# Performance work log

Hardware: AMD Instinct MI355X
Metric: run time of the kernel (lower is better)

The kernel has to match this reference:

```python
import jax, jax.numpy as jnp
import numpy as np

HEADS = 4
DIM_HEAD = 64
SCALE = 10.0
EPS = 1e-12  # matches torch F.normalize default eps


def setup_inputs() -> dict:
    key = jax.random.key(0)
    k1, k2, k3, k4, k5 = jax.random.split(key, 5)
    dim = 256
    hidden = HEADS * DIM_HEAD
    x = jax.random.normal(k1, (16, dim, 32, 32), dtype=jnp.float32)
    y = jax.random.normal(k2, (16, dim, 32, 32), dtype=jnp.float32)
    # 1x1 conv weights stored as 2D matrices (out_ch, in_ch)
    w_qkv = jax.random.normal(k3, (hidden * 3, dim), dtype=jnp.float32) * (1.0 / np.sqrt(dim))
    w_out = jax.random.normal(k4, (dim, hidden), dtype=jnp.float32) * (1.0 / np.sqrt(hidden))
    b_out = jax.random.normal(k5, (dim,), dtype=jnp.float32) * 0.01
    return {"x": x, "y": y, "w_qkv": w_qkv, "w_out": w_out, "b_out": b_out}


def _l2norm(t):
    # torch F.normalize(t, dim=-1): t / max(||t||_2, eps)
    n = jnp.sqrt(jnp.sum(t * t, axis=-1, keepdims=True))
    return t / jnp.maximum(n, EPS)


def reference(x, y, w_qkv, w_out, b_out):
    b, c, hh, ww = x.shape
    n_x = hh * ww
    n_y = y.shape[2] * y.shape[3]
    hidden = HEADS * DIM_HEAD

    # 1x1 convs == channel matmuls; only q from x and k,v from y are used
    w_q, w_k, w_v = w_qkv[:hidden], w_qkv[hidden:2 * hidden], w_qkv[2 * hidden:]
    q = jnp.einsum('oc,bcn->bon', w_q, x.reshape(b, c, n_x)).reshape(b, HEADS, DIM_HEAD, n_x)
    k = jnp.einsum('oc,bcn->bon', w_k, y.reshape(b, c, n_y)).reshape(b, HEADS, DIM_HEAD, n_y)
    v = jnp.einsum('oc,bcn->bon', w_v, y.reshape(b, c, n_y)).reshape(b, HEADS, DIM_HEAD, n_y)

    # l2norm over the spatial (last) axis, as in the source
    q = _l2norm(q)
    k = _l2norm(k)

    sim = jnp.einsum('bhdi,bhdj->bhij', q, k) * SCALE          # [b,h,n_x,n_y]
    attn = jax.nn.softmax(sim, axis=-1)
    out = jnp.einsum('bhij,bhdj->bhid', attn, v)                # [b,h,n_x,d]

    # 'b h (x y) d -> b (h d) x y'
    out = out.transpose(0, 1, 3, 2).reshape(b, hidden, hh, ww)
    out = jnp.einsum('oc,bcn->bon', w_out, out.reshape(b, hidden, n_x))
    out = out + b_out[None, :, None]
    return out.reshape(b, -1, hh, ww)
```

## Files before the change

### kernel.cpp

```cpp
#include <hip/hip_runtime.h>
#include <hip/hip_bf16.h>
#include <stdint.h>

typedef __attribute__((ext_vector_type(8))) short short8;
typedef __attribute__((ext_vector_type(4))) float f32x4;
typedef __attribute__((ext_vector_type(4))) unsigned short ushort4v;

#define MFMA16(a, b, c) __builtin_amdgcn_mfma_f32_16x16x32_bf16((a), (b), (c), 0, 0, 0)


__device__ __forceinline__ ushort f2bf(float f) {
  union { float f; unsigned u; } x; x.f = f;
  unsigned r = x.u + 0x7FFFu + ((x.u >> 16) & 1u);
  return (ushort)(r >> 16);
}

__device__ __forceinline__ short8 ld8(const ushort* p) {
  return *reinterpret_cast<const short8*>(p);
}

__device__ __forceinline__ void gll16(const void* g, void* l) {
  __builtin_amdgcn_global_load_lds(
      reinterpret_cast<const __attribute__((address_space(1))) unsigned int*>(
          reinterpret_cast<uintptr_t>(g)),
      reinterpret_cast<__attribute__((address_space(3))) unsigned int*>(
          reinterpret_cast<uintptr_t>(l)),
      16, 0, 0);
}

__global__ __launch_bounds__(256) void k_tcvt(const float* __restrict__ x,
    const float* __restrict__ y, ushort* __restrict__ xbt, ushort* __restrict__ ybt,
    const float* __restrict__ wqkv, const float* __restrict__ wout,
    ushort* __restrict__ wqkvb, ushort* __restrict__ woutb) {
  int tile = blockIdx.x;
  if (tile >= 2048) {
    const int total1 = 768 * 256;
    const int total = total1 + 256 * 256;
    for (int i = (tile - 2048) * 256 + threadIdx.x; i < total; i += 64 * 256) {
      if (i < total1) wqkvb[i] = f2bf(wqkv[i]);
      else woutb[i - total1] = f2bf(wout[i - total1]);
    }
    return;
  }
  const float* src; ushort* dst;
  if (tile >= 1024) { tile -= 1024; src = y; dst = ybt; }
  else { src = x; dst = xbt; }
  int b = tile >> 6;
  int c0 = ((tile >> 4) & 3) << 6;
  int n0 = (tile & 15) << 6;
  __shared__ ushort lds[64][65];
  int tid = threadIdx.x;
  int nl = tid & 63, cl = tid >> 6;
  const float* sb = src + ((size_t)b << 18);
#pragma unroll
  for (int s = 0; s < 16; ++s) {
    int c = cl + (s << 2);
    lds[c][nl] = f2bf(sb[(size_t)(c0 + c) * 1024 + n0 + nl]);
  }
  __syncthreads();
  ushort* db = dst + ((size_t)b << 18);
  int cl2 = tid & 63, nl2 = tid >> 6;
#pragma unroll
  for (int s = 0; s < 16; ++s) {
    int n = nl2 + (s << 2);
    db[(size_t)(n0 + n) * 256 + c0 + cl2] = lds[cl2][n];
  }
}

__global__ __launch_bounds__(512, 4) void k_qkv(const ushort* __restrict__ wqkvb,
    const ushort* __restrict__ xbt, const ushort* __restrict__ ybt,
    ushort* __restrict__ qt, ushort* __restrict__ kt, ushort* __restrict__ vbuf) {
  int bid = blockIdx.x;
  int lid = (bid & 7) * 48 + (bid >> 3);
  int ox = lid % 24;
  int b = lid / 24;
  int o0 = ox * 32;
  const ushort* Bsrc = (o0 < 256) ? xbt : ybt;
  const ushort* Bm = Bsrc + ((size_t)b << 18);
  int tid = threadIdx.x;
  int l = tid & 63, w = tid >> 6;
  int r = l & 15, g = l >> 4;
  const ushort* Ab = wqkvb + (size_t)(o0 + r) * 256 + g * 8;
  const ushort* Bb = Bm + (size_t)(w * 128 + r) * 256 + g * 8;
  f32x4 acc[2][8];
#pragma unroll
  for (int i = 0; i < 2; ++i)
#pragma unroll
    for (int j = 0; j < 8; ++j) acc[i][j] = (f32x4){0.f, 0.f, 0.f, 0.f};
#pragma unroll
  for (int ks = 0; ks < 8; ++ks) {
    short8 a0 = ld8(Ab + ks * 32);
    short8 a1 = ld8(Ab + 4096 + ks * 32);
#pragma unroll
    for (int nf = 0; nf < 8; ++nf) {
      short8 bv = ld8(Bb + (size_t)nf * 4096 + ks * 32);
      acc[0][nf] = MFMA16(a0, bv, acc[0][nf]);
      acc[1][nf] = MFMA16(a1, bv, acc[1][nf]);
    }
  }
  if (o0 < 512) {
    __shared__ float snorm[8][32];
    __shared__ float fs[32];
    float ss[2][4];
#pragma unroll
    for (int mf = 0; mf < 2; ++mf)
#pragma unroll
      for (int reg = 0; reg < 4; ++reg) {
        float s = 0.f;
#pragma unroll
        for (int nf = 0; nf < 8; ++nf) { float v = acc[mf][nf][reg]; s += v * v; }
#pragma unroll
        for (int m = 1; m < 16; m <<= 1) s += __shfl_xor(s, m);
        ss[mf][reg] = s;
      }
    if (r == 0) {
#pragma unroll
      for (int mf = 0; mf < 2; ++mf)
#pragma unroll
        for (int reg = 0; reg < 4; ++reg)
          snorm[w][mf * 16 + g * 4 + reg] = ss[mf][reg];
    }
    __syncthreads();
    if (tid < 32) {
      float s = 0.f;
#pragma unroll
      for (int w2 = 0; w2 < 8; ++w2) s += snorm[w2][tid];
      fs[tid] = ((o0 < 256) ? 10.0f : 1.0f) / fmaxf(sqrtf(s), 1e-12f);
    }
    __syncthreads();
    float fr[2][4];
#pragma unroll
    for (int mf = 0; mf < 2; ++mf)
#pragma unroll
      for (int reg = 0; reg < 4; ++reg) fr[mf][reg] = fs[mf * 16 + g * 4 + reg];
    int od = (o0 < 256) ? o0 : o0 - 256;
    int hh = od >> 6, d0 = od & 63;
    ushort* dst = ((o0 < 256) ? qt : kt) + (((size_t)(b * 4 + hh)) << 16);
#pragma unroll
    for (int mf = 0; mf < 2; ++mf)
#pragma unroll
      for (int nf = 0; nf < 8; ++nf) {
        int n = w * 128 + nf * 16 + r;
        ushort4v u;
#pragma unroll
        for (int reg = 0; reg < 4; ++reg) u[reg] = f2bf(acc[mf][nf][reg] * fr[mf][reg]);
        *reinterpret_cast<ushort4v*>(dst + (size_t)n * 64 + d0 + mf * 16 + g * 4) = u;
      }
  } else {
#pragma unroll
    for (int mf = 0; mf < 2; ++mf) {
      int ob = o0 - 512 + mf * 16 + g * 4;
#pragma unroll
      for (int nf = 0; nf < 8; ++nf) {
        int n = w * 128 + nf * 16 + r;
#pragma unroll
        for (int reg = 0; reg < 4; ++reg)
          vbuf[(((size_t)b * 256 + ob + reg) << 10) + n] = f2bf(acc[mf][nf][reg]);
      }
    }
  }
}

__global__ __launch_bounds__(512, 4) void k_attn(const ushort* __restrict__ qt,
    const ushort* __restrict__ kt, const ushort* __restrict__ vbuf,
    ushort* __restrict__ aot) {
  int hb = blockIdx.x;
  int it = blockIdx.y;
  int h = hb & 3, b = hb >> 2;
  int tid = threadIdx.x;
  int l = tid & 63, w = tid >> 6;
  int r = l & 15, g = l >> 4;
  size_t ho = ((size_t)hb) << 16;
  const ushort* Q = qt + ho;
  const char* Kg = (const char*)(kt + ho);
  const char* Vg = (const char*)(vbuf + ((size_t)b << 18) + ((size_t)h << 16));
  int i0 = it * 128 + w * 16;

  __shared__ __align__(16) ushort Kb[2][4096];
  __shared__ __align__(16) ushort Vb[2][4096];
  __shared__ __align__(16) ushort plds[8][1024];

  int L = w * 1024 + l * 16;
  int srow = L >> 7;
  int swz = (srow & 7) << 4;
  int ksrc = L ^ swz;
  int vsrc_col = (L & 127) ^ swz;

  short8 qa[2];
#pragma unroll
  for (int ks = 0; ks < 2; ++ks)
    qa[ks] = ld8(Q + (size_t)(i0 + r) * 64 + ks * 32 + g * 8);

  f32x4 oacc[4];
  float rsum[4];
#pragma unroll
  for (int j = 0; j < 4; ++j) { oacc[j] = (f32x4){0.f, 0.f, 0.f, 0.f}; rsum[j] = 0.f; }

#define STAGE(buf, j0v) do { \
    gll16(Kg + (j0v) * 128 + ksrc, (char*)&Kb[buf][0] + w * 1024); \
    gll16(Vg + (size_t)srow * 2048 + (j0v) * 2 + vsrc_col, (char*)&Vb[buf][0] + w * 1024); \
  } while (0)

  STAGE(0, 0);
  __syncthreads();

  char* plc = (char*)plds[w];
  for (int t = 0; t < 16; ++t) {
    int cur = t & 1;
    if (t < 15) STAGE(cur ^ 1, (t + 1) * 64);
    const char* Kc = (const char*)&Kb[cur][0];
    const char* Vc = (const char*)&Vb[cur][0];
    f32x4 sacc[4];
#pragma unroll
    for (int nf = 0; nf < 4; ++nf) sacc[nf] = (f32x4){0.f, 0.f, 0.f, 0.f};
#pragma unroll
    for (int nf = 0; nf < 4; ++nf) {
      int row = nf * 16 + r;
      int sw = (row & 7) << 4;
      short8 k0 = *reinterpret_cast<const short8*>(Kc + ((row * 128 + g * 16) ^ sw));
      short8 k1 = *reinterpret_cast<const short8*>(Kc + ((row * 128 + 64 + g * 16) ^ sw));
      sacc[nf] = MFMA16(qa[0], k0, sacc[nf]);
      sacc[nf] = MFMA16(qa[1], k1, sacc[nf]);
    }
#pragma unroll
    for (int nf = 0; nf < 4; ++nf)
#pragma unroll
      for (int reg = 0; reg < 4; ++reg) {
        float p = __expf(sacc[nf][reg]);
        rsum[reg] += p;
        union { float f; unsigned u; } cv; cv.f = p;
        int row = g * 4 + reg;
        int xorv = ((row ^ (row >> 3)) & 7) << 4;
        int byteo = row * 128 + (((nf * 16 + r) * 2) ^ xorv);
        *(ushort*)(plc + byteo) = (ushort)(cv.u >> 16);
      }
    short8 pa[2];
#pragma unroll
    for (int ks = 0; ks < 2; ++ks) {
      int xorv = (r ^ (r >> 3)) & 7;
      int blk = (ks * 4 + g) ^ xorv;
      pa[ks] = *reinterpret_cast<const short8*>(plc + r * 128 + blk * 16);
    }
#pragma unroll
    for (int df = 0; df < 4; ++df) {
      int row = df * 16 + r;
      int sw = (row & 7) << 4;
#pragma unroll
      for (int ks = 0; ks < 2; ++ks) {
        short8 vf = *reinterpret_cast<const short8*>(Vc + ((row * 128 + ks * 64 + g * 16) ^ sw));
        oacc[df] = MFMA16(pa[ks], vf, oacc[df]);
      }
    }
    __syncthreads();
  }
#undef STAGE

#pragma unroll
  for (int reg = 0; reg < 4; ++reg) {
    float s = rsum[reg];
#pragma unroll
    for (int m = 1; m < 16; m <<= 1) s += __shfl_xor(s, m);
    rsum[reg] = 1.0f / s;
  }
#pragma unroll
  for (int df = 0; df < 4; ++df)
#pragma unroll
    for (int reg = 0; reg < 4; ++reg) {
      int i = i0 + g * 4 + reg;
      int d = df * 16 + r;
      float vo = oacc[df][reg] * rsum[reg];
      aot[((size_t)b << 18) + (size_t)i * 256 + h * 64 + d] = f2bf(vo);
    }
}

__global__ __launch_bounds__(512, 6) void k_out(const ushort* __restrict__ woutb,
    const ushort* __restrict__ aot, const float* __restrict__ bout,
    float* __restrict__ out) {
  int bid = blockIdx.x;
  int lid = (bid & 7) * 64 + (bid >> 3);
  int ox = lid & 15;
  int t = lid >> 4;
  int nb = t & 1;
  int b = t >> 1;
  int o0 = ox * 16;
  int tid = threadIdx.x, l = tid & 63, w = tid >> 6, r = l & 15, g = l >> 4;
  const ushort* Ab = woutb + (size_t)(o0 + r) * 256 + g * 8;
  const ushort* Bb = aot + ((size_t)b << 18) + (size_t)(nb * 512 + w * 64 + r) * 256 + g * 8;
  f32x4 acc[4];
#pragma unroll
  for (int j = 0; j < 4; ++j) acc[j] = (f32x4){0.f, 0.f, 0.f, 0.f};
#pragma unroll
  for (int ks = 0; ks < 8; ++ks) {
    short8 a0 = ld8(Ab + ks * 32);
#pragma unroll
    for (int nf = 0; nf < 4; ++nf) {
      short8 bv = ld8(Bb + (size_t)nf * 4096 + ks * 32);
      acc[nf] = MFMA16(a0, bv, acc[nf]);
    }
  }
  float bias[4];
#pragma unroll
  for (int reg = 0; reg < 4; ++reg) bias[reg] = bout[o0 + g * 4 + reg];
#pragma unroll
  for (int nf = 0; nf < 4; ++nf)
#pragma unroll
    for (int reg = 0; reg < 4; ++reg) {
      size_t o = (size_t)(b * 256 + o0 + g * 4 + reg);
      out[(o << 10) + nb * 512 + w * 64 + nf * 16 + r] = acc[nf][reg] + bias[reg];
    }
}

extern "C" void kernel_launch(void* const* d_in, const int* in_sizes, int n_in,
                              void* d_out, int out_size, void* d_ws, size_t ws_size,
                              hipStream_t stream) {
  const float* x     = (const float*)d_in[0];
  const float* y     = (const float*)d_in[1];
  const float* wqkv  = (const float*)d_in[2];
  const float* wout  = (const float*)d_in[3];
  const float* bout  = (const float*)d_in[4];
  float* out = (float*)d_out;
  char* ws = (char*)d_ws;

  ushort* xbt   = (ushort*)(ws + 0ull);
  ushort* aot   = (ushort*)(ws + 0ull);
  ushort* ybt   = (ushort*)(ws + 8388608ull);
  ushort* qt    = (ushort*)(ws + 16777216ull);
  ushort* kt    = (ushort*)(ws + 25165824ull);
  ushort* vbuf  = (ushort*)(ws + 33554432ull);
  ushort* wqkvb = (ushort*)(ws + 41943040ull);
  ushort* woutb = (ushort*)(ws + 42336256ull);

  k_tcvt<<<2112, 256, 0, stream>>>(x, y, xbt, ybt, wqkv, wout, wqkvb, woutb);
  k_qkv<<<384, 512, 0, stream>>>(wqkvb, xbt, ybt, qt, kt, vbuf);
  k_attn<<<dim3(64, 8), 512, 0, stream>>>(qt, kt, vbuf, aot);
  k_out<<<512, 512, 0, stream>>>(woutb, aot, bout, out);
}
```

Measured before the change: 186.3 us.

## Stage GEMM B tiles through double-buffered LDS via direct global-to-LDS loads

The QKV and output projection kernels now preload the weight fragments into registers and stream the activation operand through a double-buffered 128 KiB LDS tile, using global_load_lds with an XOR swizzle to avoid bank conflicts. The output projection also doubles its output-channel tile to 32 and halves the grid. This replaces per-wave direct global loads of B with staged, overlapped loads, at the cost of one block per CU due to the large LDS footprint.

After: 160.8 us. 1.16x faster.

```diff
diff --git a/kernel.cpp b/kernel.cpp
--- a/kernel.cpp
+++ b/kernel.cpp
@@ -26,6 +26,13 @@
       reinterpret_cast<__attribute__((address_space(3))) unsigned int*>(
           reinterpret_cast<uintptr_t>(l)),
       16, 0, 0);
+}
+
+__device__ __forceinline__ void stage_tile(const char* gbase, char* ldsbase,
+                                           int goff, int ldsw) {
+#pragma unroll
+  for (int c = 0; c < 8; ++c)
+    gll16(gbase + c * 8192 + goff, ldsbase + c * 8192 + ldsw);
 }
 
 __global__ __launch_bounds__(256) void k_tcvt(const float* __restrict__ x,
@@ -67,7 +74,7 @@
   }
 }
 
-__global__ __launch_bounds__(512, 4) void k_qkv(const ushort* __restrict__ wqkvb,
+__global__ __launch_bounds__(512, 2) void k_qkv(const ushort* __restrict__ wqkvb,
     const ushort* __restrict__ xbt, const ushort* __restrict__ ybt,
     ushort* __restrict__ qt, ushort* __restrict__ kt, ushort* __restrict__ vbuf) {
   int bid = blockIdx.x;
@@ -76,31 +83,53 @@
   int b = lid / 24;
   int o0 = ox * 32;
   const ushort* Bsrc = (o0 < 256) ? xbt : ybt;
-  const ushort* Bm = Bsrc + ((size_t)b << 18);
+  const char* Bm = (const char*)(Bsrc + ((size_t)b << 18));
   int tid = threadIdx.x;
   int l = tid & 63, w = tid >> 6;
   int r = l & 15, g = l >> 4;
+
+  __shared__ __align__(16) char Bt[2][65536];
+  __shared__ float snorm[8][32];
+  __shared__ float fs[32];
+
   const ushort* Ab = wqkvb + (size_t)(o0 + r) * 256 + g * 8;
-  const ushort* Bb = Bm + (size_t)(w * 128 + r) * 256 + g * 8;
+  short8 areg[2][8];
+#pragma unroll
+  for (int ks = 0; ks < 8; ++ks) {
+    areg[0][ks] = ld8(Ab + ks * 32);
+    areg[1][ks] = ld8(Ab + 4096 + ks * 32);
+  }
+
+  int Lb = tid * 16;
+  int trow = Lb >> 9;
+  int goff = trow * 512 + ((Lb & 511) ^ ((trow & 7) << 4));
+  int ldsw = w * 1024;
+
   f32x4 acc[2][8];
 #pragma unroll
   for (int i = 0; i < 2; ++i)
 #pragma unroll
     for (int j = 0; j < 8; ++j) acc[i][j] = (f32x4){0.f, 0.f, 0.f, 0.f};
-#pragma unroll
-  for (int ks = 0; ks < 8; ++ks) {
-    short8 a0 = ld8(Ab + ks * 32);
-    short8 a1 = ld8(Ab + 4096 + ks * 32);
-#pragma unroll
-    for (int nf = 0; nf < 8; ++nf) {
-      short8 bv = ld8(Bb + (size_t)nf * 4096 + ks * 32);
-      acc[0][nf] = MFMA16(a0, bv, acc[0][nf]);
-      acc[1][nf] = MFMA16(a1, bv, acc[1][nf]);
-    }
-  }
+
+  stage_tile(Bm, &Bt[0][0], goff, ldsw);
+  __syncthreads();
+
+  int rr = w * 16 + r;
+  int sw = (r & 7) << 4;
+  for (int nt = 0; nt < 8; ++nt) {
+    int cur = nt & 1;
+    if (nt < 7) stage_tile(Bm + (size_t)(nt + 1) * 65536, &Bt[cur ^ 1][0], goff, ldsw);
+    const char* Bc = &Bt[cur][0];
+#pragma unroll
+    for (int ks = 0; ks < 8; ++ks) {
+      short8 bv = *reinterpret_cast<const short8*>(Bc + rr * 512 + ((ks * 64 + g * 16) ^ sw));
+      acc[0][nt] = MFMA16(areg[0][ks], bv, acc[0][nt]);
+      acc[1][nt] = MFMA16(areg[1][ks], bv, acc[1][nt]);
+    }
+    __syncthreads();
+  }
+
   if (o0 < 512) {
-    __shared__ float snorm[8][32];
-    __shared__ float fs[32];
     float ss[2][4];
 #pragma unroll
     for (int mf = 0; mf < 2; ++mf)
@@ -108,7 +137,7 @@
       for (int reg = 0; reg < 4; ++reg) {
         float s = 0.f;
 #pragma unroll
-        for (int nf = 0; nf < 8; ++nf) { float v = acc[mf][nf][reg]; s += v * v; }
+        for (int nt = 0; nt < 8; ++nt) { float v = acc[mf][nt][reg]; s += v * v; }
 #pragma unroll
         for (int m = 1; m < 16; m <<= 1) s += __shfl_xor(s, m);
         ss[mf][reg] = s;
@@ -139,11 +168,11 @@
 #pragma unroll
     for (int mf = 0; mf < 2; ++mf)
 #pragma unroll
-      for (int nf = 0; nf < 8; ++nf) {
-        int n = w * 128 + nf * 16 + r;
+      for (int nt = 0; nt < 8; ++nt) {
+        int n = nt * 128 + w * 16 + r;
         ushort4v u;
 #pragma unroll
-        for (int reg = 0; reg < 4; ++reg) u[reg] = f2bf(acc[mf][nf][reg] * fr[mf][reg]);
+        for (int reg = 0; reg < 4; ++reg) u[reg] = f2bf(acc[mf][nt][reg] * fr[mf][reg]);
         *reinterpret_cast<ushort4v*>(dst + (size_t)n * 64 + d0 + mf * 16 + g * 4) = u;
       }
   } else {
@@ -151,11 +180,11 @@
     for (int mf = 0; mf < 2; ++mf) {
       int ob = o0 - 512 + mf * 16 + g * 4;
 #pragma unroll
-      for (int nf = 0; nf < 8; ++nf) {
-        int n = w * 128 + nf * 16 + r;
+      for (int nt = 0; nt < 8; ++nt) {
+        int n = nt * 128 + w * 16 + r;
 #pragma unroll
         for (int reg = 0; reg < 4; ++reg)
-          vbuf[(((size_t)b * 256 + ob + reg) << 10) + n] = f2bf(acc[mf][nf][reg]);
+          vbuf[(((size_t)b * 256 + ob + reg) << 10) + n] = f2bf(acc[mf][nt][reg]);
       }
     }
   }
@@ -273,41 +302,73 @@
     }
 }
 
-__global__ __launch_bounds__(512, 6) void k_out(const ushort* __restrict__ woutb,
+__global__ __launch_bounds__(512, 2) void k_out(const ushort* __restrict__ woutb,
     const ushort* __restrict__ aot, const float* __restrict__ bout,
     float* __restrict__ out) {
   int bid = blockIdx.x;
-  int lid = (bid & 7) * 64 + (bid >> 3);
-  int ox = lid & 15;
-  int t = lid >> 4;
+  int lid = (bid & 7) * 32 + (bid >> 3);
+  int ox = lid & 7;
+  int t = lid >> 3;
   int nb = t & 1;
   int b = t >> 1;
-  int o0 = ox * 16;
+  int o0 = ox * 32;
   int tid = threadIdx.x, l = tid & 63, w = tid >> 6, r = l & 15, g = l >> 4;
+  const char* Bm = (const char*)(aot + ((size_t)b << 18) + ((size_t)nb << 17));
+
+  __shared__ __align__(16) char Bt[2][65536];
+
   const ushort* Ab = woutb + (size_t)(o0 + r) * 256 + g * 8;
-  const ushort* Bb = aot + ((size_t)b << 18) + (size_t)(nb * 512 + w * 64 + r) * 256 + g * 8;
-  f32x4 acc[4];
-#pragma unroll
-  for (int j = 0; j < 4; ++j) acc[j] = (f32x4){0.f, 0.f, 0.f, 0.f};
+  short8 areg[2][8];
 #pragma unroll
   for (int ks = 0; ks < 8; ++ks) {
-    short8 a0 = ld8(Ab + ks * 32);
-#pragma unroll
-    for (int nf = 0; nf < 4; ++nf) {
-      short8 bv = ld8(Bb + (size_t)nf * 4096 + ks * 32);
-      acc[nf] = MFMA16(a0, bv, acc[nf]);
-    }
-  }
-  float bias[4];
-#pragma unroll
-  for (int reg = 0; reg < 4; ++reg) bias[reg] = bout[o0 + g * 4 + reg];
-#pragma unroll
-  for (int nf = 0; nf < 4; ++nf)
-#pragma unroll
-    for (int reg = 0; reg < 4; ++reg) {
-      size_t o = (size_t)(b * 256 + o0 + g * 4 + reg);
-      out[(o << 10) + nb * 512 + w * 64 + nf * 16 + r] = acc[nf][reg] + bias[reg];
-    }
+    areg[0][ks] = ld8(Ab + ks * 32);
+    areg[1][ks] = ld8(Ab + 4096 + ks * 32);
+  }
+
+  int Lb = tid * 16;
+  int trow = Lb >> 9;
+  int goff = trow * 512 + ((Lb & 511) ^ ((trow & 7) << 4));
+  int ldsw = w * 1024;
+
+  f32x4 acc[2][4];
+#pragma unroll
+  for (int i = 0; i < 2; ++i)
+#pragma unroll
+    for (int j = 0; j < 4; ++j) acc[i][j] = (f32x4){0.f, 0.f, 0.f, 0.f};
+
+  stage_tile(Bm, &Bt[0][0], goff, ldsw);
+  __syncthreads();
+
+  int rr = w * 16 + r;
+  int sw = (r & 7) << 4;
+  for (int nt = 0; nt < 4; ++nt) {
+    int cur = nt & 1;
+    if (nt < 3) stage_tile(Bm + (size_t)(nt + 1) * 65536, &Bt[cur ^ 1][0], goff, ldsw);
+    const char* Bc = &Bt[cur][0];
+#pragma unroll
+    for (int ks = 0; ks < 8; ++ks) {
+      short8 bv = *reinterpret_cast<const short8*>(Bc + rr * 512 + ((ks * 64 + g * 16) ^ sw));
+      acc[0][nt] = MFMA16(areg[0][ks], bv, acc[0][nt]);
+      acc[1][nt] = MFMA16(areg[1][ks], bv, acc[1][nt]);
+    }
+    __syncthreads();
+  }
+
+  float bias[2][4];
+#pragma unroll
+  for (int mf = 0; mf < 2; ++mf)
+#pragma unroll
+    for (int reg = 0; reg < 4; ++reg) bias[mf][reg] = bout[o0 + mf * 16 + g * 4 + reg];
+#pragma unroll
+  for (int mf = 0; mf < 2; ++mf)
+#pragma unroll
+    for (int nt = 0; nt < 4; ++nt)
+#pragma unroll
+      for (int reg = 0; reg < 4; ++reg) {
+        size_t o = (size_t)(b * 256 + o0 + mf * 16 + g * 4 + reg);
+        int n = nb * 512 + nt * 128 + w * 16 + r;
+        out[(o << 10) + n] = acc[mf][nt][reg] + bias[mf][reg];
+      }
 }
 
 extern "C" void kernel_launch(void* const* d_in, const int* in_sizes, int n_in,
@@ -333,5 +394,5 @@
   k_tcvt<<<2112, 256, 0, stream>>>(x, y, xbt, ybt, wqkv, wout, wqkvb, woutb);
   k_qkv<<<384, 512, 0, stream>>>(wqkvb, xbt, ybt, qt, kt, vbuf);
   k_attn<<<dim3(64, 8), 512, 0, stream>>>(qt, kt, vbuf, aot);
-  k_out<<<512, 512, 0, stream>>>(woutb, aot, bout, out);
-}
+  k_out<<<256, 512, 0, stream>>>(woutb, aot, bout, out);
+}
```
